# Performance work log

Hardware: AMD Instinct MI355X
Metric: run time of the kernel (lower is better)

The kernel has to match this reference:

```python
import jax, jax.numpy as jnp
import numpy as np

KS = 3
N_TAPS = KS * KS
PAD = 1
EPS = 1e-5


def conv2d(x, w, b=None, stride=1, padding=1):
    out = jax.lax.conv_general_dilated(
        x, w, (stride, stride), [(padding, padding), (padding, padding)],
        dimension_numbers=('NCHW', 'OIHW', 'NCHW'))
    if b is not None:
        out = out + b[None, :, None, None]
    return out


def deform_conv(x, p_conv_w, p_conv_b, dcn_w):
    # x: (b,c,H,W). Canonical pure-torch DCNv1 (no modulation), stride=1, padding=1.
    off = conv2d(x, p_conv_w, p_conv_b, 1, 1).transpose(0, 2, 3, 1)  # (b,h,w,2N)
    b, h, w, _ = off.shape
    xp = jnp.pad(x, ((0, 0), (0, 0), (PAD, PAD), (PAD, PAD)))  # zero-pad
    Hp, Wp = xp.shape[2], xp.shape[3]
    r = jnp.arange(-(KS - 1) // 2, (KS - 1) // 2 + 1, dtype=x.dtype)
    pn_h, pn_w = [a.reshape(-1) for a in jnp.meshgrid(r, r, indexing='ij')]  # (N,)
    p0_h = jnp.arange(1, h + 1, dtype=x.dtype)[:, None, None]  # (h,1,1)
    p0_w = jnp.arange(1, w + 1, dtype=x.dtype)[None, :, None]  # (1,w,1)
    ph = jnp.clip(p0_h + pn_h + off[..., :N_TAPS], 0, Hp - 1)   # (b,h,w,N)
    pw = jnp.clip(p0_w + pn_w + off[..., N_TAPS:], 0, Wp - 1)
    fh, fw = jnp.floor(ph), jnp.floor(pw)
    lt_h = jnp.clip(fh, 0, Hp - 1); lt_w = jnp.clip(fw, 0, Wp - 1)
    rb_h = jnp.clip(fh + 1, 0, Hp - 1); rb_w = jnp.clip(fw + 1, 0, Wp - 1)
    g_lt = (1 + (lt_h - ph)) * (1 + (lt_w - pw))
    g_rb = (1 - (rb_h - ph)) * (1 - (rb_w - pw))
    g_lb = (1 + (lt_h - ph)) * (1 - (rb_w - pw))
    g_rt = (1 - (rb_h - ph)) * (1 + (lt_w - pw))
    ilt_h, ilt_w = lt_h.astype(jnp.int32), lt_w.astype(jnp.int32)
    irb_h, irb_w = rb_h.astype(jnp.int32), rb_w.astype(jnp.int32)
    gather = jax.vmap(lambda im, iy, ix: im[:, iy, ix])  # per-sample -> (c,h,w,N)
    x_lt = gather(xp, ilt_h, ilt_w)
    x_rb = gather(xp, irb_h, irb_w)
    x_lb = gather(xp, ilt_h, irb_w)
    x_rt = gather(xp, irb_h, ilt_w)
    xo = (g_lt[:, None] * x_lt + g_rb[:, None] * x_rb +
          g_lb[:, None] * x_lb + g_rt[:, None] * x_rt)  # (b,c,h,w,N)
    O, C = dcn_w.shape[0], dcn_w.shape[1]
    # reshape-to-(h*ks,w*ks) + stride-ks conv == contraction over tap n = ky*ks+kx
    return jnp.einsum('bchwn,ocn->bohw', xo, dcn_w.reshape(O, C, N_TAPS))


def batchnorm(x, gamma, beta):
    mu = x.mean((0, 2, 3), keepdims=True)
    var = ((x - mu) ** 2).mean((0, 2, 3), keepdims=True)  # biased var (torch BN)
    return gamma[None, :, None, None] * (x - mu) * jax.lax.rsqrt(var + EPS) + beta[None, :, None, None]


def setup_inputs() -> dict:
    key = jax.random.key(0)
    ks = jax.random.split(key, 8)
    B, C, O, H, W = 8, 64, 128, 128, 128
    return {
        'x': jax.random.normal(ks[0], (B, C, H, W), jnp.float32),
        'p_conv_w': jax.random.normal(ks[1], (2 * N_TAPS, C, 3, 3), jnp.float32) * 0.01,
        'p_conv_b': jax.random.normal(ks[2], (2 * N_TAPS,), jnp.float32) * 0.1,
        'dcn_w': jax.random.normal(ks[3], (C, C, 3, 3), jnp.float32) * 0.05,
        'bn_gamma': jnp.ones((C,), jnp.float32) + 0.1 * jax.random.normal(ks[4], (C,), jnp.float32),
        'bn_beta': 0.1 * jax.random.normal(ks[5], (C,), jnp.float32),
        'conv2_w': jax.random.normal(ks[6], (O, C, 3, 3), jnp.float32) * 0.05,
        'conv2_b': jax.random.normal(ks[7], (O,), jnp.float32) * 0.05,
    }


def reference(x, p_conv_w, p_conv_b, dcn_w, bn_gamma, bn_beta, conv2_w, conv2_b):
    out = deform_conv(x, p_conv_w, p_conv_b, dcn_w)
    out = jax.nn.relu(batchnorm(out, bn_gamma, bn_beta))
    out = out + x
    return conv2d(out, conv2_w, conv2_b, 1, 1)  # (B, 128, 128, 128)
```

## Files before the change

kernel.cpp:

```cpp
#include <hip/hip_runtime.h>
#include <hip/hip_bf16.h>

#define BB 8
#define CC 64
#define OO 128
#define HH 128
#define WW 128
#define HW (HH*WW)
#define NTAP 9

typedef float f32x4 __attribute__((ext_vector_type(4)));
typedef short short8 __attribute__((ext_vector_type(8)));

__device__ __forceinline__ uint f2bf(float v) {
    uint b = __float_as_uint(v);
    return (b + 0x7FFFu + ((b >> 16) & 1u)) >> 16;
}

__device__ __forceinline__ float sampf(const float* __restrict__ xc, int iy, int ix) {
    unsigned uy = (unsigned)(iy - 1), ux = (unsigned)(ix - 1);
    return (uy < 128u && ux < 128u) ? xc[uy * 128 + ux] : 0.f;
}

__global__ void k_repack(const float* __restrict__ pw, const float* __restrict__ dw,
                         const float* __restrict__ cw,
                         float* __restrict__ wp1, float* __restrict__ wpd,
                         ushort* __restrict__ wb2) {
    int i = blockIdx.x * 256 + threadIdx.x;
    if (i < 10368) {
        int o = i % 18, t = (i / 18) % 9, c = i / 162;
        wp1[i] = pw[(o * 64 + c) * 9 + t];
    }
    if (i < 36864) {
        int o = i % 64, t = (i / 64) % 9, c = i / 576;
        wpd[i] = dw[(o * 64 + c) * 9 + t];
    }
    if (i < 73728) {
        int j = i & 7, lane = (i >> 3) & 63, ot = (i >> 9) & 7;
        int kc = (i >> 12) & 1, t = i >> 13;
        int c = kc * 32 + (lane >> 4) * 8 + j;
        int oc = ot * 16 + (lane & 15);
        wb2[i] = (ushort)f2bf(cw[(oc * 64 + c) * 9 + t]);
    }
}

__global__ __launch_bounds__(256) void k_pconv(const float* __restrict__ x,
                                               const float* __restrict__ wp1,
                                               const float* __restrict__ pb,
                                               float* __restrict__ off) {
    int tile = blockIdx.x;
    int b = blockIdx.y;
    int ty0 = (tile >> 3) * 8, tx0 = (tile & 7) * 16;
    int tid = threadIdx.x;
    int px = tid & 127;
    int ch = __builtin_amdgcn_readfirstlane(tid >> 7);
    int pyr = px >> 4, pxl = px & 15;

    __shared__ float lx[32][180];
    __shared__ float pacc[128][19];

    float acc[18];
#pragma unroll
    for (int o = 0; o < 18; o++) acc[o] = 0.f;

    for (int h = 0; h < 2; h++) {
        __syncthreads();
        for (int idx = tid; idx < 5760; idx += 256) {
            int c = idx / 180, pos = idx % 180;
            int r = pos / 18, col = pos % 18;
            int gy = ty0 + r - 1, gx = tx0 + col - 1;
            float v = 0.f;
            if ((unsigned)gy < 128u && (unsigned)gx < 128u)
                v = x[((b * 64 + h * 32 + c) * 128 + gy) * 128 + gx];
            lx[c][pos] = v;
        }
        __syncthreads();
        for (int ci = 0; ci < 16; ci++) {
            int c = ch * 16 + ci;
#pragma unroll
            for (int t = 0; t < 9; t++) {
                float xv = lx[c][(pyr + t / 3) * 18 + pxl + t % 3];
                const float* wr = wp1 + ((h * 32 + c) * 9 + t) * 18;
#pragma unroll
                for (int o = 0; o < 18; o++) acc[o] = fmaf(xv, wr[o], acc[o]);
            }
        }
    }
    if (ch == 1) {
#pragma unroll
        for (int o = 0; o < 18; o++) pacc[px][o] = acc[o];
    }
    __syncthreads();
    if (ch == 0) {
        int yy = ty0 + pyr, xx = tx0 + pxl;
#pragma unroll
        for (int o = 0; o < 18; o++)
            off[((b * 18 + o) * 128 + yy) * 128 + xx] = acc[o] + pacc[px][o] + pb[o];
    }
}

__global__ __launch_bounds__(256) void k_deform(const float* __restrict__ x,
                                                const float* __restrict__ off,
                                                const float* __restrict__ wpd,
                                                float* __restrict__ y) {
    int tile = blockIdx.x;
    int b = blockIdx.y;
    int ty0 = (tile / 16) * 8, tx0 = (tile % 16) * 8;
    int tid = threadIdx.x;

    __shared__ uint   mwin[576];
    __shared__ float4 mwt[576];
    __shared__ uint   xtile[4 * 256];
    __shared__ uint   xo[4][580];

    for (int e = tid; e < 576; e += 256) {
        int n = e >> 6, p = e & 63;
        int py = p >> 3, px = p & 7;
        int yy = ty0 + py, xx = tx0 + px;
        float offh = off[((b * 18 + n) * 128 + yy) * 128 + xx];
        float offw = off[((b * 18 + 9 + n) * 128 + yy) * 128 + xx];
        float ph = (float)(yy + 1) + (float)(n / 3 - 1) + offh;
        float pw = (float)(xx + 1) + (float)(n % 3 - 1) + offw;
        ph = fminf(fmaxf(ph, 0.f), 129.f);
        pw = fminf(fmaxf(pw, 0.f), 129.f);
        float fh = floorf(ph), fw = floorf(pw);
        int lth = (int)fh, ltw = (int)fw;
        int rbh = min(lth + 1, 129), rbw = min(ltw + 1, 129);
        float dh_l = 1.f + (fh - ph);
        float dh_r = 1.f - ((float)rbh - ph);
        float dw_l = 1.f + (fw - pw);
        float dw_r = 1.f - ((float)rbw - pw);
        int uy0 = lth - 1, ux0 = ltw - 1, uy1 = rbh - 1, ux1 = rbw - 1;
        bool iy0 = (unsigned)uy0 < 128u, ix0 = (unsigned)ux0 < 128u;
        bool iy1 = (unsigned)uy1 < 128u, ix1 = (unsigned)ux1 < 128u;
        float w_lt = (iy0 && ix0) ? dh_l * dw_l : 0.f;
        float w_rb = (iy1 && ix1) ? dh_r * dw_r : 0.f;
        float w_lb = (iy0 && ix1) ? dh_l * dw_r : 0.f;
        float w_rt = (iy1 && ix0) ? dh_r * dw_l : 0.f;
        mwt[e] = make_float4(w_lt, w_rb, w_lb, w_rt);
        int wy0 = uy0 - ty0 + 4, wx0 = ux0 - tx0 + 4;
        int wy1 = uy1 - ty0 + 4, wx1 = ux1 - tx0 + 4;
        uint win = 0xFFFFFFFFu;
        if ((unsigned)wy0 < 16u && (unsigned)wx0 < 16u &&
            (unsigned)wy1 < 16u && (unsigned)wx1 < 16u) {
            uint o00 = (uint)(wy0 * 16 + wx0);
            uint o11 = (uint)(wy1 * 16 + wx1);
            uint o01 = (uint)(wy0 * 16 + wx1);
            uint o10 = (uint)(wy1 * 16 + wx0);
            win = o00 | (o11 << 8) | (o01 << 16) | (o10 << 24);
        }
        mwin[e] = win;
    }

    float acc[16] = {};
    int cg = tid >> 6;
    int l64 = tid & 63;
    int cgoff = cg * 256;
    int ob = __builtin_amdgcn_readfirstlane(cg * 16);

    int sgy = ty0 - 4 + (tid >> 4), sgx = tx0 - 4 + (tid & 15);
    bool sinb = ((unsigned)sgy < 128u && (unsigned)sgx < 128u);
    int spos = sgy * 128 + sgx;

    for (int cc = 0; cc < 8; cc++) {
#pragma unroll
        for (int q = 0; q < 4; q++) {
            int c0 = cc * 8 + 2 * q;
            float v0 = 0.f, v1 = 0.f;
            if (sinb) {
                v0 = x[(size_t)(b * 64 + c0) * HW + spos];
                v1 = x[(size_t)(b * 64 + c0 + 1) * HW + spos];
            }
            xtile[q * 256 + tid] = (f2bf(v1) << 16) | f2bf(v0);
        }
        __syncthreads();
#pragma unroll 2
        for (int i = 0; i < 9; i++) {
            int e = l64 + 64 * i;
            uint w = mwin[e];
            float4 g = mwt[e];
            float vlo, vhi;
            if (__builtin_expect(w != 0xFFFFFFFFu, 1)) {
                uint u00 = xtile[cgoff + (w & 255u)];
                uint u11 = xtile[cgoff + ((w >> 8) & 255u)];
                uint u01 = xtile[cgoff + ((w >> 16) & 255u)];
                uint u10 = xtile[cgoff + (w >> 24)];
                float a00l = __uint_as_float(u00 << 16), a00h = __uint_as_float(u00 & 0xFFFF0000u);
                float a11l = __uint_as_float(u11 << 16), a11h = __uint_as_float(u11 & 0xFFFF0000u);
                float a01l = __uint_as_float(u01 << 16), a01h = __uint_as_float(u01 & 0xFFFF0000u);
                float a10l = __uint_as_float(u10 << 16), a10h = __uint_as_float(u10 & 0xFFFF0000u);
                vlo = g.x * a00l + g.y * a11l + g.z * a01l + g.w * a10l;
                vhi = g.x * a00h + g.y * a11h + g.z * a01h + g.w * a10h;
            } else {
                int n = e >> 6, p = e & 63;
                int yy2 = ty0 + (p >> 3), xx2 = tx0 + (p & 7);
                float offh = off[((b * 18 + n) * 128 + yy2) * 128 + xx2];
                float offw = off[((b * 18 + 9 + n) * 128 + yy2) * 128 + xx2];
                float ph = fminf(fmaxf((float)(yy2 + 1) + (float)(n / 3 - 1) + offh, 0.f), 129.f);
                float pw = fminf(fmaxf((float)(xx2 + 1) + (float)(n % 3 - 1) + offw, 0.f), 129.f);
                int lth = (int)floorf(ph), ltw = (int)floorf(pw);
                int rbh = min(lth + 1, 129), rbw = min(ltw + 1, 129);
                const float* xc0 = x + (size_t)(b * 64 + cc * 8 + 2 * cg) * HW;
                const float* xc1 = xc0 + HW;
                vlo = g.x * sampf(xc0, lth, ltw) + g.y * sampf(xc0, rbh, rbw)
                    + g.z * sampf(xc0, lth, rbw) + g.w * sampf(xc0, rbh, ltw);
                vhi = g.x * sampf(xc1, lth, ltw) + g.y * sampf(xc1, rbh, rbw)
                    + g.z * sampf(xc1, lth, rbw) + g.w * sampf(xc1, rbh, ltw);
            }
            xo[cg][e] = (f2bf(vhi) << 16) | f2bf(vlo);
        }
        __syncthreads();
        for (int q = 0; q < 4; q++) {
#pragma unroll
            for (int n = 0; n < 9; n++) {
                uint u = xo[q][n * 64 + l64];
                float xlo = __uint_as_float(u << 16);
                float xhi = __uint_as_float(u & 0xFFFF0000u);
                const float* w0 = wpd + (((cc * 8 + 2 * q) * 9 + n) * 64) + ob;
                const float* w1 = w0 + 576;
#pragma unroll
                for (int j = 0; j < 16; j++) acc[j] = fmaf(xlo, w0[j], acc[j]);
#pragma unroll
                for (int j = 0; j < 16; j++) acc[j] = fmaf(xhi, w1[j], acc[j]);
            }
        }
        __syncthreads();
    }

    int yy = ty0 + (l64 >> 3), xx = tx0 + (l64 & 7);
#pragma unroll
    for (int j = 0; j < 16; j++)
        y[(size_t)(b * 64 + ob + j) * HW + yy * 128 + xx] = acc[j];
}

__global__ __launch_bounds__(256) void k_bnpart(const float* __restrict__ y,
                                                float* __restrict__ part) {
    int c = blockIdx.x;
    int bq = blockIdx.y;
    int b = bq >> 2, hq = bq & 3;
    int tid = threadIdx.x;
    const float4* p = (const float4*)(y + (size_t)(b * 64 + c) * HW + hq * 4096);
    float s = 0.f, sq = 0.f;
    for (int i = tid; i < 1024; i += 256) {
        float4 v = p[i];
        s += v.x + v.y + v.z + v.w;
        sq += v.x * v.x + v.y * v.y + v.z * v.z + v.w * v.w;
    }
#pragma unroll
    for (int o = 32; o > 0; o >>= 1) {
        s += __shfl_down(s, o);
        sq += __shfl_down(sq, o);
    }
    __shared__ float rs[4], rq[4];
    int wid = tid >> 6;
    if ((tid & 63) == 0) { rs[wid] = s; rq[wid] = sq; }
    __syncthreads();
    if (tid == 0) {
        part[((b * 64 + c) * 4 + hq) * 2]     = rs[0] + rs[1] + rs[2] + rs[3];
        part[((b * 64 + c) * 4 + hq) * 2 + 1] = rq[0] + rq[1] + rq[2] + rq[3];
    }
}

__global__ void k_bnfinal(const float* __restrict__ part,
                          const float* __restrict__ gamma,
                          const float* __restrict__ beta,
                          float* __restrict__ ss) {
    int c = threadIdx.x;
    float s = 0.f, sq = 0.f;
#pragma unroll
    for (int b = 0; b < 8; b++)
#pragma unroll
        for (int hq = 0; hq < 4; hq++) {
            s += part[((b * 64 + c) * 4 + hq) * 2];
            sq += part[((b * 64 + c) * 4 + hq) * 2 + 1];
        }
    const float inv = 1.f / (float)(8 * HW);
    float mean = s * inv;
    float var = sq * inv - mean * mean;
    float scale = gamma[c] * rsqrtf(var + 1e-5f);
    ss[c] = scale;
    ss[64 + c] = beta[c] - mean * scale;
}

__global__ __launch_bounds__(256) void k_conv2(const float* __restrict__ x,
                                               const float* __restrict__ y,
                                               const float* __restrict__ ss,
                                               const ushort* __restrict__ wb2,
                                               const float* __restrict__ b2,
                                               float* __restrict__ out) {
    int tile = blockIdx.x, b = blockIdx.y;
    int ty0 = (tile / 16) * 8, tx0 = (tile % 16) * 8;
    int tid = threadIdx.x;

    __shared__ uint lz[3600];

    for (int idx = tid; idx < 3200; idx += 256) {
        int q = idx / 100, pos = idx % 100;
        int r = pos / 10, col = pos % 10;
        int gy = ty0 + r - 1, gx = tx0 + col - 1;
        uint u = 0;
        if ((unsigned)gy < 128u && (unsigned)gx < 128u) {
            int c0 = q * 2;
            int gi = ((b * 64 + c0) * HW) + gy * 128 + gx;
            float t0 = fmaf(y[gi], ss[c0], ss[64 + c0]);
            float v0 = fmaxf(t0, 0.f) + x[gi];
            float t1 = fmaf(y[gi + HW], ss[c0 + 1], ss[65 + c0]);
            float v1 = fmaxf(t1, 0.f) + x[gi + HW];
            u = (f2bf(v1) << 16) | f2bf(v0);
        }
        lz[pos * 36 + q] = u;
    }
    __syncthreads();

    int lane = tid & 63, pg = tid >> 6;
    int r16 = lane & 15, jg = lane >> 4;
    int p = pg * 16 + r16;
    int pyA = p >> 3, pxA = p & 7;

    f32x4 acc[8];
#pragma unroll
    for (int ot = 0; ot < 8; ot++) {
        float bv = b2[ot * 16 + r16];
        acc[ot] = (f32x4){bv, bv, bv, bv};
    }

#pragma unroll
    for (int t = 0; t < 9; t++) {
        int pos = (pyA + t / 3) * 10 + (pxA + t % 3);
#pragma unroll
        for (int kc = 0; kc < 2; kc++) {
            short8 av = *(const short8*)(lz + pos * 36 + kc * 16 + jg * 4);
            const ushort* wk = wb2 + (t * 2 + kc) * 4096 + lane * 8;
#pragma unroll
            for (int ot = 0; ot < 8; ot++) {
                short8 bv = *(const short8*)(wk + ot * 512);
                acc[ot] = __builtin_amdgcn_mfma_f32_16x16x32_bf16(av, bv, acc[ot], 0, 0, 0);
            }
        }
    }

    int p0 = pg * 16 + jg * 4;
    int yy = ty0 + (p0 >> 3), xx = tx0 + (p0 & 7);
#pragma unroll
    for (int ot = 0; ot < 8; ot++) {
        int oc = ot * 16 + r16;
        *(f32x4*)(out + (size_t)(b * 128 + oc) * HW + yy * 128 + xx) = acc[ot];
    }
}

extern "C" void kernel_launch(void* const* d_in, const int* in_sizes, int n_in,
                              void* d_out, int out_size, void* d_ws, size_t ws_size,
                              hipStream_t stream) {
    const float* x     = (const float*)d_in[0];
    const float* pw    = (const float*)d_in[1];
    const float* pb    = (const float*)d_in[2];
    const float* dw    = (const float*)d_in[3];
    const float* gamma = (const float*)d_in[4];
    const float* beta  = (const float*)d_in[5];
    const float* cw    = (const float*)d_in[6];
    const float* cb    = (const float*)d_in[7];
    float* out = (float*)d_out;
    float* ws  = (float*)d_ws;

    float*  wp1  = ws;
    float*  ss   = ws + 10368;
    float*  part = ws + 10496;
    float*  wpd  = ws + 14592;
    ushort* wb2  = (ushort*)(ws + 51456);
    float*  off  = ws + 88320;
    float*  yb   = ws + 2447616;

    k_repack<<<dim3(288), dim3(256), 0, stream>>>(pw, dw, cw, wp1, wpd, wb2);
    k_pconv<<<dim3(128, 8), dim3(256), 0, stream>>>(x, wp1, pb, off);
    k_deform<<<dim3(256, 8), dim3(256), 0, stream>>>(x, off, wpd, yb);
    k_bnpart<<<dim3(64, 32), dim3(256), 0, stream>>>(yb, part);
    k_bnfinal<<<dim3(1), dim3(64), 0, stream>>>(part, gamma, beta, ss);
    k_conv2<<<dim3(256, 8), dim3(256), 0, stream>>>(x, yb, ss, wb2, cb, out);
}
```

Before: 319.1 us.

## Split conv2 MFMA work by output-channel group per wave instead of pixel group

Each wave in the final conv kernel used to own 16 pixels and all 128 output channels, so every wave read the full bf16 weight slice from global memory for each tap. Now each wave owns 32 output channels across all 64 pixels of the tile. It loads only 2 weight fragments per tap and chunk and reads 4 activation fragments from LDS. This cuts global and L2 weight traffic per wave fourfold, at the cost of more LDS reads and more address arithmetic per MFMA.

```diff
diff --git a/kernel.cpp b/kernel.cpp
--- a/kernel.cpp
+++ b/kernel.cpp
@@ -312,39 +312,45 @@
     }
     __syncthreads();
 
-    int lane = tid & 63, pg = tid >> 6;
+    int lane = tid & 63, wv = tid >> 6;
     int r16 = lane & 15, jg = lane >> 4;
-    int p = pg * 16 + r16;
-    int pyA = p >> 3, pxA = p & 7;
-
-    f32x4 acc[8];
-#pragma unroll
-    for (int ot = 0; ot < 8; ot++) {
-        float bv = b2[ot * 16 + r16];
-        acc[ot] = (f32x4){bv, bv, bv, bv};
+
+    f32x4 acc[4][2];
+#pragma unroll
+    for (int otl = 0; otl < 2; otl++) {
+        float bv = b2[(2 * wv + otl) * 16 + r16];
+#pragma unroll
+        for (int pgx = 0; pgx < 4; pgx++)
+            acc[pgx][otl] = (f32x4){bv, bv, bv, bv};
     }
 
 #pragma unroll
     for (int t = 0; t < 9; t++) {
-        int pos = (pyA + t / 3) * 10 + (pxA + t % 3);
 #pragma unroll
         for (int kc = 0; kc < 2; kc++) {
-            short8 av = *(const short8*)(lz + pos * 36 + kc * 16 + jg * 4);
             const ushort* wk = wb2 + (t * 2 + kc) * 4096 + lane * 8;
-#pragma unroll
-            for (int ot = 0; ot < 8; ot++) {
-                short8 bv = *(const short8*)(wk + ot * 512);
-                acc[ot] = __builtin_amdgcn_mfma_f32_16x16x32_bf16(av, bv, acc[ot], 0, 0, 0);
-            }
-        }
-    }
-
-    int p0 = pg * 16 + jg * 4;
-    int yy = ty0 + (p0 >> 3), xx = tx0 + (p0 & 7);
-#pragma unroll
-    for (int ot = 0; ot < 8; ot++) {
-        int oc = ot * 16 + r16;
-        *(f32x4*)(out + (size_t)(b * 128 + oc) * HW + yy * 128 + xx) = acc[ot];
+            short8 bv0 = *(const short8*)(wk + (2 * wv) * 512);
+            short8 bv1 = *(const short8*)(wk + (2 * wv + 1) * 512);
+#pragma unroll
+            for (int pgx = 0; pgx < 4; pgx++) {
+                int p = pgx * 16 + r16;
+                int pos = ((p >> 3) + t / 3) * 10 + ((p & 7) + t % 3);
+                short8 av = *(const short8*)(lz + pos * 36 + kc * 16 + jg * 4);
+                acc[pgx][0] = __builtin_amdgcn_mfma_f32_16x16x32_bf16(av, bv0, acc[pgx][0], 0, 0, 0);
+                acc[pgx][1] = __builtin_amdgcn_mfma_f32_16x16x32_bf16(av, bv1, acc[pgx][1], 0, 0, 0);
+            }
+        }
+    }
+
+#pragma unroll
+    for (int pgx = 0; pgx < 4; pgx++) {
+        int p0 = pgx * 16 + jg * 4;
+        int yy = ty0 + (p0 >> 3), xx = tx0 + (p0 & 7);
+#pragma unroll
+        for (int otl = 0; otl < 2; otl++) {
+            int oc = (2 * wv + otl) * 16 + r16;
+            *(f32x4*)(out + (size_t)(b * 128 + oc) * HW + yy * 128 + xx) = acc[pgx][otl];
+        }
     }
 }
 
```

Measured after the change: 313.3 us, median of 2. About the same (-1.8%).
